# Performance work log

Hardware: AMD Instinct MI355X
Metric: run time of the kernel (lower is better)

The kernel has to match this reference:

```python
import jax, jax.numpy as jnp
import numpy as np

NUM_HEADS = 16
NUM_KV_HEADS = 4
HEAD_DIM = 128
BASE_THETA = 10000.0


def _rope_cos_sin(seq_len, head_dim, dtype):
    # standard (ntk_alpha=1) rotate-half RoPE tables: [S, head_dim]
    inv_freq = 1.0 / (BASE_THETA ** (jnp.arange(0, head_dim, 2, dtype=jnp.float32) / head_dim))
    angles = jnp.arange(seq_len, dtype=jnp.float32)[:, None] * inv_freq[None, :]  # [S, D/2]
    cos = jnp.concatenate([jnp.cos(angles), jnp.cos(angles)], axis=-1).astype(dtype)
    sin = jnp.concatenate([jnp.sin(angles), jnp.sin(angles)], axis=-1).astype(dtype)
    return cos, sin


def _rotate_half(t):
    half = t.shape[-1] // 2
    return jnp.concatenate([-t[..., half:], t[..., :half]], axis=-1)


def setup_inputs() -> dict:
    key = jax.random.key(0)
    ks = jax.random.split(key, 5)
    B, S, E = 2, 2048, 2048
    KV = NUM_KV_HEADS * HEAD_DIM  # 512
    scale = 0.02
    return {
        "x": jax.random.normal(ks[0], (B, S, E), dtype=jnp.float32),
        "Wq": jax.random.normal(ks[1], (E, E), dtype=jnp.float32) * scale,
        "Wk": jax.random.normal(ks[2], (E, KV), dtype=jnp.float32) * scale,
        "Wv": jax.random.normal(ks[3], (E, KV), dtype=jnp.float32) * scale,
        "Wo": jax.random.normal(ks[4], (E, E), dtype=jnp.float32) * scale,
    }


def reference(x, Wq, Wk, Wv, Wo):
    B, S, E = x.shape
    n_rep = NUM_HEADS // NUM_KV_HEADS
    scale = 1.0 / jnp.sqrt(jnp.float32(HEAD_DIM))

    # QKV projections (bias=False)
    q = (x @ Wq).reshape(B, S, NUM_HEADS, HEAD_DIM)
    k = (x @ Wk).reshape(B, S, NUM_KV_HEADS, HEAD_DIM)
    v = (x @ Wv).reshape(B, S, NUM_KV_HEADS, HEAD_DIM)

    # dynamic RoPE on q, k
    cos, sin = _rope_cos_sin(S, HEAD_DIM, x.dtype)
    cos = cos[None, :, None, :]
    sin = sin[None, :, None, :]
    q = q * cos + _rotate_half(q) * sin
    k = k * cos + _rotate_half(k) * sin

    # GQA: repeat kv heads to match query heads
    k = jnp.repeat(k, n_rep, axis=2)
    v = jnp.repeat(v, n_rep, axis=2)

    # [B, H, S, D]
    q = q.transpose(0, 2, 1, 3)
    k = k.transpose(0, 2, 1, 3)
    v = v.transpose(0, 2, 1, 3)

    # causal mask (window_size=0 -> standard causal, additive float mask)
    i = jnp.arange(S)[:, None]
    j = jnp.arange(S)[None, :]
    neg = jnp.finfo(jnp.float32).min
    causal = jnp.where(j > i, neg, 0.0).astype(jnp.float32)  # [S, S]

    scores = jnp.einsum("bhqd,bhkd->bhqk", q, k) * scale
    scores = scores + causal[None, None, :, :]
    weights = jax.nn.softmax(scores.astype(jnp.float32), axis=-1)
    attn = jnp.einsum("bhqk,bhkd->bhqd", weights.astype(v.dtype), v)

    attn = attn.transpose(0, 2, 1, 3).reshape(B, S, E)
    return attn @ Wo
```

## Files before the change

kernel.cpp:

```cpp
#include <hip/hip_runtime.h>
#include <math.h>


typedef __attribute__((ext_vector_type(8))) short short8;
typedef __attribute__((ext_vector_type(4))) float f32x4;
typedef __attribute__((ext_vector_type(16))) float f32x16;

typedef const __attribute__((address_space(1))) void* gvp;
typedef __attribute__((address_space(3))) void* svp;

__device__ __forceinline__ void async16(const void* g, void* l) {
  __builtin_amdgcn_global_load_lds((gvp)g, (svp)l, 16, 0, 0);
}
__device__ __forceinline__ void wait_vm0() { asm volatile("s_waitcnt vmcnt(0)" ::: "memory"); }
__device__ __forceinline__ void barrier_raw() { asm volatile("s_barrier" ::: "memory"); }

__device__ __forceinline__ unsigned short f2b(float f) {
  unsigned int u = __builtin_bit_cast(unsigned int, f);
  u += 0x7fffu + ((u >> 16) & 1u);
  return (unsigned short)(u >> 16);
}
__device__ __forceinline__ float b2f(unsigned short h) {
  unsigned int u = ((unsigned int)h) << 16;
  return __builtin_bit_cast(float, u);
}

__device__ __forceinline__ unsigned int pk_bf16(float a, float b) {
  unsigned int r;
  asm("v_cvt_pk_bf16_f32 %0, %1, %2" : "=v"(r) : "v"(a), "v"(b));
  return r;
}
__device__ __forceinline__ void plswap(unsigned int& a, unsigned int& b) {
  asm("v_permlane32_swap_b32 %0, %1" : "+v"(a), "+v"(b));
}

__global__ __launch_bounds__(256) void convx(const float* __restrict__ x,
                                             unsigned short* __restrict__ xb) {
  int i = blockIdx.x * 256 + threadIdx.x;
  const float4* p = (const float4*)x + (size_t)i * 2;
  float4 a = p[0], b4 = p[1];
  union { short8 v; unsigned short u[8]; } o;
  o.u[0] = f2b(a.x);  o.u[1] = f2b(a.y);  o.u[2] = f2b(a.z);  o.u[3] = f2b(a.w);
  o.u[4] = f2b(b4.x); o.u[5] = f2b(b4.y); o.u[6] = f2b(b4.z); o.u[7] = f2b(b4.w);
  ((short8*)xb)[i] = o.v;
}

__global__ __launch_bounds__(256) void wconv_all(const float* __restrict__ Wq,
                                                 const float* __restrict__ Wk,
                                                 const float* __restrict__ Wv,
                                                 const float* __restrict__ Wo,
                                                 unsigned short* __restrict__ WqkvT,
                                                 unsigned short* __restrict__ WoT) {
  __shared__ float t[32][33];
  int idx = blockIdx.x;
  const float* W; unsigned short* WT; int N, tx, ty;
  const int K = 2048;
  if (idx < 4096)      { W = Wq; WT = WqkvT;                         N = 2048; idx -= 0;    tx = idx & 63; ty = idx >> 6; }
  else if (idx < 5120) { W = Wk; WT = WqkvT + (size_t)2048 * 2048;   N = 512;  idx -= 4096; tx = idx & 15; ty = idx >> 4; }
  else if (idx < 6144) { W = Wv; WT = WqkvT + (size_t)2560 * 2048;   N = 512;  idx -= 5120; tx = idx & 15; ty = idx >> 4; }
  else                 { W = Wo; WT = WoT;                           N = 2048; idx -= 6144; tx = idx & 63; ty = idx >> 6; }
  int c = threadIdx.x & 31, r0 = threadIdx.x >> 5;
  int k0 = ty * 32, n0 = tx * 32;
#pragma unroll
  for (int r = r0; r < 32; r += 8) t[r][c] = W[(size_t)(k0 + r) * N + n0 + c];
  __syncthreads();
#pragma unroll
  for (int r = r0; r < 32; r += 8) WT[(size_t)(n0 + r) * K + k0 + c] = f2b(t[c][r]);
}

__global__ __launch_bounds__(256) void gemm_bt(const unsigned short* __restrict__ A,
                                               const unsigned short* __restrict__ BT,
                                               void* __restrict__ Cout,
                                               int M, int N, int K, int out_bf16) {
  const int n0 = blockIdx.x * 128;
  const int m0 = blockIdx.y * 128;
  const int tid = threadIdx.x;
  const int w = tid >> 6, lane = tid & 63, l15 = lane & 15, quad = lane >> 4;
  const int wm = w >> 1, wn = w & 1;

  __shared__ __align__(16) unsigned short As[2][128 * 64];
  __shared__ __align__(16) unsigned short Bs[2][128 * 64];

  f32x4 acc[4][4];
#pragma unroll
  for (int mi = 0; mi < 4; mi++)
#pragma unroll
    for (int ni = 0; ni < 4; ni++) acc[mi][ni] = (f32x4){0.f, 0.f, 0.f, 0.f};

  const int rl = lane >> 3;
  const int cl = lane & 7;
  const unsigned short* Ab = A + (size_t)m0 * K;
  const unsigned short* Bb = BT + (size_t)n0 * K;

#pragma unroll
  for (int i = 0; i < 4; i++) {
    int row = w * 32 + i * 8 + rl;
    int gc = cl ^ (row & 7);
    async16(Ab + (size_t)row * K + gc * 8, &As[0][(w * 32 + i * 8) * 64]);
    async16(Bb + (size_t)row * K + gc * 8, &Bs[0][(w * 32 + i * 8) * 64]);
  }

  const int nIter = K >> 6;
  for (int j = 0; j < nIter; j++) {
    wait_vm0();
    barrier_raw();
    const int cur = j & 1;

    if (j + 1 < nIter) {
      int kb = (j + 1) * 64;
#pragma unroll
      for (int i = 0; i < 4; i++) {
        int row = w * 32 + i * 8 + rl;
        int gc = cl ^ (row & 7);
        async16(Ab + (size_t)row * K + kb + gc * 8, &As[cur ^ 1][(w * 32 + i * 8) * 64]);
        async16(Bb + (size_t)row * K + kb + gc * 8, &Bs[cur ^ 1][(w * 32 + i * 8) * 64]);
      }
    }

    const unsigned short* as = &As[cur][0];
    const unsigned short* bs = &Bs[cur][0];
#pragma unroll
    for (int kk = 0; kk < 2; kk++) {
      short8 af[4], bfv[4];
#pragma unroll
      for (int mi = 0; mi < 4; mi++) {
        int row = wm * 64 + mi * 16 + l15;
        af[mi] = *(const short8*)&as[row * 64 + (((kk * 4 + quad) ^ (row & 7)) * 8)];
      }
#pragma unroll
      for (int ni = 0; ni < 4; ni++) {
        int row = wn * 64 + ni * 16 + l15;
        bfv[ni] = *(const short8*)&bs[row * 64 + (((kk * 4 + quad) ^ (row & 7)) * 8)];
      }
#pragma unroll
      for (int mi = 0; mi < 4; mi++)
#pragma unroll
        for (int ni = 0; ni < 4; ni++)
          acc[mi][ni] = __builtin_amdgcn_mfma_f32_16x16x32_bf16(af[mi], bfv[ni],
                                                                acc[mi][ni], 0, 0, 0);
    }
  }

  if (out_bf16) {
    unsigned short* C = (unsigned short*)Cout;
#pragma unroll
    for (int mi = 0; mi < 4; mi++)
#pragma unroll
      for (int ni = 0; ni < 4; ni++)
#pragma unroll
        for (int r = 0; r < 4; r++) {
          int row = m0 + wm * 64 + mi * 16 + quad * 4 + r;
          int col = n0 + wn * 64 + ni * 16 + l15;
          C[(size_t)row * N + col] = f2b(acc[mi][ni][r]);
        }
  } else {
    float* C = (float*)Cout;
#pragma unroll
    for (int mi = 0; mi < 4; mi++)
#pragma unroll
      for (int ni = 0; ni < 4; ni++)
#pragma unroll
        for (int r = 0; r < 4; r++) {
          int row = m0 + wm * 64 + mi * 16 + quad * 4 + r;
          int col = n0 + wn * 64 + ni * 16 + l15;
          C[(size_t)row * N + col] = acc[mi][ni][r];
        }
  }
}

#define SC_TOT 0.12753785056274918f
__global__ __launch_bounds__(256) void rope_kernel(const unsigned short* __restrict__ qkv,
                                                   unsigned short* __restrict__ Q,
                                                   unsigned short* __restrict__ Kd) {
  int b = blockIdx.z, hh = blockIdx.y;
  int tid = threadIdx.x;
  int d = tid & 63, sl = tid >> 6;
  int s = blockIdx.x * 4 + sl;
  const unsigned short* src = qkv + ((size_t)(b * 2048 + s)) * 3072 + hh * 128;
  float lo = b2f(src[d]), hi = b2f(src[d + 64]);
  float invf = exp2f(-0.20762050593046f * (float)d);
  float ang = (float)s * invf;
  float sn, cs;
  sincosf(ang, &sn, &cs);
  float nlo = lo * cs - hi * sn;
  float nhi = hi * cs + lo * sn;
  unsigned short* dst;
  if (hh < 16) {
    nlo *= SC_TOT; nhi *= SC_TOT;
    dst = Q + ((size_t)((b * 16 + hh) * 2048 + s)) * 128;
  } else {
    dst = Kd + ((size_t)((b * 4 + (hh - 16)) * 2048 + s)) * 128;
  }
  dst[d] = f2b(nlo);
  dst[d + 64] = f2b(nhi);
}

__global__ __launch_bounds__(256) void vtrans(const unsigned short* __restrict__ qkv,
                                              unsigned short* __restrict__ Vt) {
  int bkv = blockIdx.z;
  int b = bkv >> 2, kv = bkv & 3;
  int s0 = blockIdx.x * 64, d0 = blockIdx.y * 64;
  __shared__ unsigned short t[64][65];
  int c = threadIdx.x & 63, r0 = threadIdx.x >> 6;
  const unsigned short* src = qkv + ((size_t)(b * 2048 + s0)) * 3072 + 2560 + kv * 128 + d0;
#pragma unroll
  for (int r = r0; r < 64; r += 4) t[r][c] = src[(size_t)r * 3072 + c];
  __syncthreads();
  unsigned short* dst = Vt + ((size_t)bkv * 128 + d0) * 2048 + s0;
#pragma unroll
  for (int r = r0; r < 64; r += 4) dst[(size_t)r * 2048 + c] = t[c][r];
}

#define FIXED_M 12.0f

__device__ __forceinline__ void proc_acc(const f32x16& s, bool msk, int kvb, int q,
                                         float& l_own, short8& paL, short8& paH) {
  float p[16];
#pragma unroll
  for (int r = 0; r < 16; r++) {
    float v = exp2f(s[r] - FIXED_M);
    if (msk) {
      int kv = kvb + (r & 3) + 8 * (r >> 2);
      if (kv > q) v = 0.f;
    }
    p[r] = v;
    l_own += v;
  }
  unsigned int u0 = pk_bf16(p[0], p[1]),  u1 = pk_bf16(p[2], p[3]);
  unsigned int u2 = pk_bf16(p[4], p[5]),  u3 = pk_bf16(p[6], p[7]);
  plswap(u0, u2); plswap(u1, u3);
  unsigned int w0 = pk_bf16(p[8], p[9]),  w1 = pk_bf16(p[10], p[11]);
  unsigned int w2 = pk_bf16(p[12], p[13]), w3 = pk_bf16(p[14], p[15]);
  plswap(w0, w2); plswap(w1, w3);
  union { unsigned int u[4]; short8 s8; } a, b;
  a.u[0] = u0; a.u[1] = u1; a.u[2] = u2; a.u[3] = u3;
  b.u[0] = w0; b.u[1] = w1; b.u[2] = w2; b.u[3] = w3;
  paL = a.s8; paH = b.s8;
}

__global__ __launch_bounds__(512, 2) void flash2(const unsigned short* __restrict__ Q,
                                                 const unsigned short* __restrict__ Kc,
                                                 const unsigned short* __restrict__ Vt,
                                                 unsigned short* __restrict__ attn) {
  const int pair = blockIdx.x;
  const int h = blockIdx.y;
  const int b = blockIdx.z;
  const int kvh = h >> 2;
  const int tid = threadIdx.x;
  const int w = tid >> 6;
  const int g = w >> 2;
  const int wg = w & 3;
  const int lane = tid & 63;
  const int l31 = lane & 31, hi = lane >> 5, x7 = l31 & 7;

  __shared__ __align__(16) unsigned short kbuf[2][2][64 * 128];
  __shared__ __align__(16) unsigned short vbuf[2][2][128 * 64];
  __shared__ float lx[2][4][32];
  __shared__ float li[2][4][32];

  const unsigned short* Qb = Q  + ((size_t)(b * 16 + h)) * 2048 * 128;
  const unsigned short* Kb = Kc + ((size_t)(b * 4 + kvh)) * 2048 * 128;
  const unsigned short* Vb = Vt + ((size_t)(b * 4 + kvh)) * 128 * 2048;

  for (int t = 0; t < 2; t++) {
    const int qt = (t == 0) ? pair : (15 - pair);
    const int q0 = qt * 128;
    const int qw = q0 + wg * 32;
    const int qv = qw + l31;
    const int half = qt + 1;
    const int j0 = g * half;

    short8 qf[8];
    {
      const unsigned short* qp = Qb + (size_t)qv * 128 + hi * 8;
#pragma unroll
      for (int s = 0; s < 8; s++) qf[s] = *(const short8*)(qp + s * 16);
    }

    f32x16 o[4];
#pragma unroll
    for (int d = 0; d < 4; d++)
#pragma unroll
      for (int e = 0; e < 16; e++) o[d][e] = 0.f;
    float l_own = 0.f;

    __syncthreads();

#pragma unroll
    for (int k2 = 0; k2 < 4; k2++) {
      int m = wg * 4 + k2;
      int rl = m * 4 + (lane >> 4);
      int c8 = (lane & 15) ^ (rl & 7);
      async16(Kb + (size_t)(j0 * 64 + rl) * 128 + c8 * 8, &kbuf[g][0][m * 512]);
    }
#pragma unroll
    for (int k2 = 0; k2 < 4; k2++) {
      int m = wg * 4 + k2;
      int d = m * 8 + (lane >> 3);
      int c3 = (lane & 7) ^ (d & 7);
      async16(Vb + (size_t)d * 2048 + j0 * 64 + c3 * 8, &vbuf[g][0][m * 512]);
    }

    for (int i = 0; i < half; i++) {
      wait_vm0();
      barrier_raw();
      const int cur = i & 1;
      const int kb = (j0 + i) * 64;

      if (i + 1 < half) {
        int kb2 = kb + 64;
#pragma unroll
        for (int k2 = 0; k2 < 4; k2++) {
          int m = wg * 4 + k2;
          int rl = m * 4 + (lane >> 4);
          int c8 = (lane & 15) ^ (rl & 7);
          async16(Kb + (size_t)(kb2 + rl) * 128 + c8 * 8, &kbuf[g][cur ^ 1][m * 512]);
        }
#pragma unroll
        for (int k2 = 0; k2 < 4; k2++) {
          int m = wg * 4 + k2;
          int d = m * 8 + (lane >> 3);
          int c3 = (lane & 7) ^ (d & 7);
          async16(Vb + (size_t)d * 2048 + kb2 + c3 * 8, &vbuf[g][cur ^ 1][m * 512]);
        }
      }

      if (kb <= qw + 31) {
        f32x16 sA, sB;
#pragma unroll
        for (int e = 0; e < 16; e++) { sA[e] = 0.f; sB[e] = 0.f; }
        const unsigned short* kp = &kbuf[g][cur][0];
        __builtin_amdgcn_s_setprio(1);
#pragma unroll
        for (int s = 0; s < 8; s++) {
          int ch = (((s << 1) | hi) ^ x7) << 3;
          short8 ka = *(const short8*)&kp[l31 * 128 + ch];
          short8 kB2 = *(const short8*)&kp[(32 + l31) * 128 + ch];
          sA = __builtin_amdgcn_mfma_f32_32x32x16_bf16(ka, qf[s], sA, 0, 0, 0);
          sB = __builtin_amdgcn_mfma_f32_32x32x16_bf16(kB2, qf[s], sB, 0, 0, 0);
        }
        __builtin_amdgcn_s_setprio(0);

        const bool msk = (kb + 63 > qw);
        short8 pa[4];
        proc_acc(sA, msk, kb + 4 * hi, qv, l_own, pa[0], pa[1]);
        proc_acc(sB, msk, kb + 32 + 4 * hi, qv, l_own, pa[2], pa[3]);

        const unsigned short* vp = &vbuf[g][cur][0];
        __builtin_amdgcn_s_setprio(1);
#pragma unroll
        for (int db = 0; db < 4; db++) {
          int ro = (db * 32 + l31) * 64;
#pragma unroll
          for (int f = 0; f < 4; f++) {
            int ch = (((f << 1) | hi) ^ x7) << 3;
            short8 vf = *(const short8*)&vp[ro + ch];
            o[db] = __builtin_amdgcn_mfma_f32_32x32x16_bf16(pa[f], vf, o[db], 0, 0, 0);
          }
        }
        __builtin_amdgcn_s_setprio(0);
      }
    }

    __syncthreads();
    {
      float* wout = (float*)&kbuf[g ^ 1][0][0];
      float lown = l_own + __shfl_xor(l_own, 32);
      if (hi == 0) lx[g][wg][l31] = lown;
      const int base = wg * 2048 + lane * 4;
      if (g == 0) {
#pragma unroll
        for (int r4 = 0; r4 < 4; r4++) {
          *(f32x4*)&wout[base + 0 * 1024 + r4 * 256] =
            (f32x4){ o[2][r4 * 4 + 0], o[2][r4 * 4 + 1], o[2][r4 * 4 + 2], o[2][r4 * 4 + 3] };
          *(f32x4*)&wout[base + 1 * 1024 + r4 * 256] =
            (f32x4){ o[3][r4 * 4 + 0], o[3][r4 * 4 + 1], o[3][r4 * 4 + 2], o[3][r4 * 4 + 3] };
        }
      } else {
#pragma unroll
        for (int r4 = 0; r4 < 4; r4++) {
          *(f32x4*)&wout[base + 0 * 1024 + r4 * 256] =
            (f32x4){ o[0][r4 * 4 + 0], o[0][r4 * 4 + 1], o[0][r4 * 4 + 2], o[0][r4 * 4 + 3] };
          *(f32x4*)&wout[base + 1 * 1024 + r4 * 256] =
            (f32x4){ o[1][r4 * 4 + 0], o[1][r4 * 4 + 1], o[1][r4 * 4 + 2], o[1][r4 * 4 + 3] };
        }
      }
      __syncthreads();
      const float* rin = (const float*)&kbuf[g][0][0];
      float ltot = lown + lx[g ^ 1][wg][l31];
      if (hi == 0) li[g][wg][l31] = 1.f / ltot;
      f32x4 inv4[4];
#pragma unroll
      for (int tt = 0; tt < 4; tt++) inv4[tt] = *(const f32x4*)&li[g][wg][tt * 8 + 4 * hi];

      unsigned short* ap0 = attn + ((size_t)(b * 2048 + qw)) * 2048 + h * 128 + l31;
      if (g == 0) {
#pragma unroll
        for (int r4 = 0; r4 < 4; r4++) {
          f32x4 v0 = *(const f32x4*)&rin[base + 0 * 1024 + r4 * 256];
          f32x4 v1 = *(const f32x4*)&rin[base + 1 * 1024 + r4 * 256];
#pragma unroll
          for (int k = 0; k < 4; k++) {
            o[0][r4 * 4 + k] += v0[k];
            o[1][r4 * 4 + k] += v1[k];
          }
        }
#pragma unroll
        for (int r = 0; r < 16; r++) {
          int rowq = (r & 3) + 8 * (r >> 2) + 4 * hi;
          float iv = inv4[r >> 2][r & 3];
          ap0[(size_t)rowq * 2048 + 0]  = f2b(o[0][r] * iv);
          ap0[(size_t)rowq * 2048 + 32] = f2b(o[1][r] * iv);
        }
      } else {
#pragma unroll
        for (int r4 = 0; r4 < 4; r4++) {
          f32x4 v0 = *(const f32x4*)&rin[base + 0 * 1024 + r4 * 256];
          f32x4 v1 = *(const f32x4*)&rin[base + 1 * 1024 + r4 * 256];
#pragma unroll
          for (int k = 0; k < 4; k++) {
            o[2][r4 * 4 + k] += v0[k];
            o[3][r4 * 4 + k] += v1[k];
          }
        }
#pragma unroll
        for (int r = 0; r < 16; r++) {
          int rowq = (r & 3) + 8 * (r >> 2) + 4 * hi;
          float iv = inv4[r >> 2][r & 3];
          ap0[(size_t)rowq * 2048 + 64] = f2b(o[2][r] * iv);
          ap0[(size_t)rowq * 2048 + 96] = f2b(o[3][r] * iv);
        }
      }
    }
  }
}

extern "C" void kernel_launch(void* const* d_in, const int* in_sizes, int n_in,
                              void* d_out, int out_size, void* d_ws, size_t ws_size,
                              hipStream_t stream) {
  const float* x  = (const float*)d_in[0];
  const float* Wq = (const float*)d_in[1];
  const float* Wk = (const float*)d_in[2];
  const float* Wv = (const float*)d_in[3];
  const float* Wo = (const float*)d_in[4];
  float* out = (float*)d_out;

  char* ws = (char*)d_ws;
  unsigned short* xb    = (unsigned short*)(ws);
  unsigned short* WqkvT = (unsigned short*)(ws + 16777216);
  unsigned short* WoT   = (unsigned short*)(ws + 29360128);
  unsigned short* qkv   = (unsigned short*)(ws + 37748736);
  unsigned short* Qm    = (unsigned short*)(ws + 62914560);
  unsigned short* Km    = (unsigned short*)(ws + 79691776);
  unsigned short* Vtm   = (unsigned short*)(ws + 83886080);
  unsigned short* attn  = xb;

  convx<<<4096, 256, 0, stream>>>(x, xb);
  wconv_all<<<10240, 256, 0, stream>>>(Wq, Wk, Wv, Wo, WqkvT, WoT);

  gemm_bt<<<dim3(24, 32), 256, 0, stream>>>(xb, WqkvT, qkv, 4096, 3072, 2048, 1);

  rope_kernel<<<dim3(512, 20, 2), 256, 0, stream>>>(qkv, Qm, Km);
  vtrans<<<dim3(32, 2, 8), 256, 0, stream>>>(qkv, Vtm);

  flash2<<<dim3(8, 16, 2), 512, 0, stream>>>(Qm, Km, Vtm, attn);

  gemm_bt<<<dim3(16, 32), 256, 0, stream>>>(attn, WoT, out, 4096, 2048, 2048, 0);
}
```

Before: 312.6 us.

## Enlarge GEMM tiles to 256x256 with 8-wave ping-pong MFMA schedule

The bf16 GEMM now uses 256x256 output tiles with 512 threads (8 waves, 2x4 layout) instead of 128x128 with 4 waves. Each wave holds a 128x64 accumulator, and the inner loop runs as four quadrant phases that alternate LDS fragment loads with MFMA bursts. The bursts are separated by barriers and raised with s_setprio, so waves interleave memory and matrix work. The larger tile raises data reuse per LDS byte. The trade-off is far fewer blocks: 192 for QKV and 128 for the output projection on a 256-CU part, which may leave compute units idle. It also raises register pressure and adds extra barriers.

```diff
diff --git a/kernel.cpp b/kernel.cpp
--- a/kernel.cpp
+++ b/kernel.cpp
@@ -68,100 +68,120 @@
   for (int r = r0; r < 32; r += 8) WT[(size_t)(n0 + r) * K + k0 + c] = f2b(t[c][r]);
 }
 
-__global__ __launch_bounds__(256) void gemm_bt(const unsigned short* __restrict__ A,
-                                               const unsigned short* __restrict__ BT,
-                                               void* __restrict__ Cout,
-                                               int M, int N, int K, int out_bf16) {
-  const int n0 = blockIdx.x * 128;
-  const int m0 = blockIdx.y * 128;
+__global__ __launch_bounds__(512, 2) void gemm_bt(const unsigned short* __restrict__ A,
+                                                  const unsigned short* __restrict__ BT,
+                                                  void* __restrict__ Cout,
+                                                  int M, int N, int K, int out_bf16) {
+  const int n0 = blockIdx.x * 256;
+  const int m0 = blockIdx.y * 256;
   const int tid = threadIdx.x;
   const int w = tid >> 6, lane = tid & 63, l15 = lane & 15, quad = lane >> 4;
-  const int wm = w >> 1, wn = w & 1;
-
-  __shared__ __align__(16) unsigned short As[2][128 * 64];
-  __shared__ __align__(16) unsigned short Bs[2][128 * 64];
-
-  f32x4 acc[4][4];
-#pragma unroll
-  for (int mi = 0; mi < 4; mi++)
+  const int wm = w >> 2, wn = w & 3;
+  const int rl = lane >> 3, cl = lane & 7;
+
+  __shared__ __align__(16) unsigned short As[2][256 * 64];
+  __shared__ __align__(16) unsigned short Bs[2][256 * 64];
+
+  f32x4 acc[8][4];
+#pragma unroll
+  for (int mi = 0; mi < 8; mi++)
 #pragma unroll
     for (int ni = 0; ni < 4; ni++) acc[mi][ni] = (f32x4){0.f, 0.f, 0.f, 0.f};
 
-  const int rl = lane >> 3;
-  const int cl = lane & 7;
   const unsigned short* Ab = A + (size_t)m0 * K;
   const unsigned short* Bb = BT + (size_t)n0 * K;
 
-#pragma unroll
-  for (int i = 0; i < 4; i++) {
-    int row = w * 32 + i * 8 + rl;
-    int gc = cl ^ (row & 7);
-    async16(Ab + (size_t)row * K + gc * 8, &As[0][(w * 32 + i * 8) * 64]);
-    async16(Bb + (size_t)row * K + gc * 8, &Bs[0][(w * 32 + i * 8) * 64]);
+#define G_STAGE(KB, BUF)                                                      \
+  { _Pragma("unroll") for (int i = 0; i < 4; ++i) {                           \
+      int row = w * 32 + i * 8 + rl;                                          \
+      int gc = cl ^ (row & 7);                                                \
+      async16(Ab + (size_t)row * K + (KB) + gc * 8,                           \
+              &As[BUF][(w * 32 + i * 8) * 64]);                               \
+      async16(Bb + (size_t)row * K + (KB) + gc * 8,                           \
+              &Bs[BUF][(w * 32 + i * 8) * 64]); } }
+
+#define LOAD_A(MH)                                                            \
+  { _Pragma("unroll") for (int mi = 0; mi < 4; ++mi) {                        \
+      int row = wm * 128 + (MH) * 64 + mi * 16 + l15;                         \
+      _Pragma("unroll") for (int kk = 0; kk < 2; ++kk)                        \
+        a8[mi][kk] = *(const short8*)&as_[row * 64 +                          \
+                        (((kk * 4 + quad) ^ (row & 7)) * 8)]; } }
+
+#define LOAD_B(NH)                                                            \
+  { _Pragma("unroll") for (int ni = 0; ni < 2; ++ni) {                        \
+      int row = wn * 64 + (NH) * 32 + ni * 16 + l15;                          \
+      _Pragma("unroll") for (int kk = 0; kk < 2; ++kk)                        \
+        b4[ni][kk] = *(const short8*)&bs_[row * 64 +                          \
+                        (((kk * 4 + quad) ^ (row & 7)) * 8)]; } }
+
+#define MFMA_C(MH, NH)                                                        \
+  { __builtin_amdgcn_s_setprio(1);                                            \
+    _Pragma("unroll") for (int mi = 0; mi < 4; ++mi)                          \
+      _Pragma("unroll") for (int ni = 0; ni < 2; ++ni)                        \
+        _Pragma("unroll") for (int kk = 0; kk < 2; ++kk)                      \
+          acc[(MH) * 4 + mi][(NH) * 2 + ni] =                                 \
+            __builtin_amdgcn_mfma_f32_16x16x32_bf16(                          \
+              a8[mi][kk], b4[ni][kk],                                         \
+              acc[(MH) * 4 + mi][(NH) * 2 + ni], 0, 0, 0);                    \
+    __builtin_amdgcn_s_setprio(0); }
+
+  G_STAGE(0, 0);
+  wait_vm0();
+  barrier_raw();
+
+  const int nIter = K >> 6;
+  short8 a8[4][2], b4[2][2];
+  for (int j = 0; j < nIter; ++j) {
+    const int cur = j & 1;
+    if (j + 1 < nIter) G_STAGE((j + 1) * 64, cur ^ 1);
+    const unsigned short* as_ = &As[cur][0];
+    const unsigned short* bs_ = &Bs[cur][0];
+
+    LOAD_A(0); LOAD_B(0);
+    barrier_raw();
+    MFMA_C(0, 0);
+    barrier_raw();
+    LOAD_B(1);
+    barrier_raw();
+    MFMA_C(0, 1);
+    barrier_raw();
+    LOAD_A(1);
+    barrier_raw();
+    MFMA_C(1, 1);
+    barrier_raw();
+    LOAD_B(0);
+    barrier_raw();
+    MFMA_C(1, 0);
+    wait_vm0();
+    barrier_raw();
   }
 
-  const int nIter = K >> 6;
-  for (int j = 0; j < nIter; j++) {
-    wait_vm0();
-    barrier_raw();
-    const int cur = j & 1;
-
-    if (j + 1 < nIter) {
-      int kb = (j + 1) * 64;
-#pragma unroll
-      for (int i = 0; i < 4; i++) {
-        int row = w * 32 + i * 8 + rl;
-        int gc = cl ^ (row & 7);
-        async16(Ab + (size_t)row * K + kb + gc * 8, &As[cur ^ 1][(w * 32 + i * 8) * 64]);
-        async16(Bb + (size_t)row * K + kb + gc * 8, &Bs[cur ^ 1][(w * 32 + i * 8) * 64]);
-      }
-    }
-
-    const unsigned short* as = &As[cur][0];
-    const unsigned short* bs = &Bs[cur][0];
-#pragma unroll
-    for (int kk = 0; kk < 2; kk++) {
-      short8 af[4], bfv[4];
-#pragma unroll
-      for (int mi = 0; mi < 4; mi++) {
-        int row = wm * 64 + mi * 16 + l15;
-        af[mi] = *(const short8*)&as[row * 64 + (((kk * 4 + quad) ^ (row & 7)) * 8)];
-      }
-#pragma unroll
-      for (int ni = 0; ni < 4; ni++) {
-        int row = wn * 64 + ni * 16 + l15;
-        bfv[ni] = *(const short8*)&bs[row * 64 + (((kk * 4 + quad) ^ (row & 7)) * 8)];
-      }
-#pragma unroll
-      for (int mi = 0; mi < 4; mi++)
-#pragma unroll
-        for (int ni = 0; ni < 4; ni++)
-          acc[mi][ni] = __builtin_amdgcn_mfma_f32_16x16x32_bf16(af[mi], bfv[ni],
-                                                                acc[mi][ni], 0, 0, 0);
-    }
-  }
+#undef G_STAGE
+#undef LOAD_A
+#undef LOAD_B
+#undef MFMA_C
 
   if (out_bf16) {
     unsigned short* C = (unsigned short*)Cout;
 #pragma unroll
-    for (int mi = 0; mi < 4; mi++)
+    for (int mi = 0; mi < 8; mi++)
 #pragma unroll
       for (int ni = 0; ni < 4; ni++)
 #pragma unroll
         for (int r = 0; r < 4; r++) {
-          int row = m0 + wm * 64 + mi * 16 + quad * 4 + r;
+          int row = m0 + wm * 128 + mi * 16 + quad * 4 + r;
           int col = n0 + wn * 64 + ni * 16 + l15;
           C[(size_t)row * N + col] = f2b(acc[mi][ni][r]);
         }
   } else {
     float* C = (float*)Cout;
 #pragma unroll
-    for (int mi = 0; mi < 4; mi++)
+    for (int mi = 0; mi < 8; mi++)
 #pragma unroll
       for (int ni = 0; ni < 4; ni++)
 #pragma unroll
         for (int r = 0; r < 4; r++) {
-          int row = m0 + wm * 64 + mi * 16 + quad * 4 + r;
+          int row = m0 + wm * 128 + mi * 16 + quad * 4 + r;
           int col = n0 + wn * 64 + ni * 16 + l15;
           C[(size_t)row * N + col] = acc[mi][ni][r];
         }
@@ -458,12 +478,12 @@
   convx<<<4096, 256, 0, stream>>>(x, xb);
   wconv_all<<<10240, 256, 0, stream>>>(Wq, Wk, Wv, Wo, WqkvT, WoT);
 
-  gemm_bt<<<dim3(24, 32), 256, 0, stream>>>(xb, WqkvT, qkv, 4096, 3072, 2048, 1);
+  gemm_bt<<<dim3(12, 16), 512, 0, stream>>>(xb, WqkvT, qkv, 4096, 3072, 2048, 1);
 
   rope_kernel<<<dim3(512, 20, 2), 256, 0, stream>>>(qkv, Qm, Km);
   vtrans<<<dim3(32, 2, 8), 256, 0, stream>>>(qkv, Vtm);
 
   flash2<<<dim3(8, 16, 2), 512, 0, stream>>>(Qm, Km, Vtm, attn);
 
-  gemm_bt<<<dim3(16, 32), 256, 0, stream>>>(attn, WoT, out, 4096, 2048, 2048, 0);
-}
+  gemm_bt<<<dim3(8, 16), 512, 0, stream>>>(attn, WoT, out, 4096, 2048, 2048, 0);
+}
```

Result: slower. 351.9 us (+12.6%).

## Fuse RoPE and V transpose into QKV GEMM epilogue; merge prep kernels

Applied to the files above, without the earlier changes.

A dedicated QKV GEMM now stages its 128x128 fp32 tile in LDS and applies RoPE (for Q/K heads) or writes the transposed V layout directly. This removes the intermediate qkv buffer round trip and two separate kernel launches. The x and weight conversion kernels are also merged into one launch. The epilogue adds LDS traffic and sincos work inside the GEMM blocks. The V output is written with scattered 2-byte stores.

```diff
diff --git a/kernel.cpp b/kernel.cpp
--- a/kernel.cpp
+++ b/kernel.cpp
@@ -34,25 +34,26 @@
   asm("v_permlane32_swap_b32 %0, %1" : "+v"(a), "+v"(b));
 }
 
-__global__ __launch_bounds__(256) void convx(const float* __restrict__ x,
-                                             unsigned short* __restrict__ xb) {
-  int i = blockIdx.x * 256 + threadIdx.x;
-  const float4* p = (const float4*)x + (size_t)i * 2;
-  float4 a = p[0], b4 = p[1];
-  union { short8 v; unsigned short u[8]; } o;
-  o.u[0] = f2b(a.x);  o.u[1] = f2b(a.y);  o.u[2] = f2b(a.z);  o.u[3] = f2b(a.w);
-  o.u[4] = f2b(b4.x); o.u[5] = f2b(b4.y); o.u[6] = f2b(b4.z); o.u[7] = f2b(b4.w);
-  ((short8*)xb)[i] = o.v;
-}
-
-__global__ __launch_bounds__(256) void wconv_all(const float* __restrict__ Wq,
-                                                 const float* __restrict__ Wk,
-                                                 const float* __restrict__ Wv,
-                                                 const float* __restrict__ Wo,
-                                                 unsigned short* __restrict__ WqkvT,
-                                                 unsigned short* __restrict__ WoT) {
+__global__ __launch_bounds__(256) void prep(const float* __restrict__ x,
+                                            const float* __restrict__ Wq,
+                                            const float* __restrict__ Wk,
+                                            const float* __restrict__ Wv,
+                                            const float* __restrict__ Wo,
+                                            unsigned short* __restrict__ xb,
+                                            unsigned short* __restrict__ WqkvT,
+                                            unsigned short* __restrict__ WoT) {
   __shared__ float t[32][33];
-  int idx = blockIdx.x;
+  if (blockIdx.x < 4096) {
+    int i = blockIdx.x * 256 + threadIdx.x;
+    const float4* p = (const float4*)x + (size_t)i * 2;
+    float4 a = p[0], b4 = p[1];
+    union { short8 v; unsigned short u[8]; } o;
+    o.u[0] = f2b(a.x);  o.u[1] = f2b(a.y);  o.u[2] = f2b(a.z);  o.u[3] = f2b(a.w);
+    o.u[4] = f2b(b4.x); o.u[5] = f2b(b4.y); o.u[6] = f2b(b4.z); o.u[7] = f2b(b4.w);
+    ((short8*)xb)[i] = o.v;
+    return;
+  }
+  int idx = blockIdx.x - 4096;
   const float* W; unsigned short* WT; int N, tx, ty;
   const int K = 2048;
   if (idx < 4096)      { W = Wq; WT = WqkvT;                         N = 2048; idx -= 0;    tx = idx & 63; ty = idx >> 6; }
@@ -169,46 +170,135 @@
 }
 
 #define SC_TOT 0.12753785056274918f
-__global__ __launch_bounds__(256) void rope_kernel(const unsigned short* __restrict__ qkv,
-                                                   unsigned short* __restrict__ Q,
-                                                   unsigned short* __restrict__ Kd) {
-  int b = blockIdx.z, hh = blockIdx.y;
-  int tid = threadIdx.x;
-  int d = tid & 63, sl = tid >> 6;
-  int s = blockIdx.x * 4 + sl;
-  const unsigned short* src = qkv + ((size_t)(b * 2048 + s)) * 3072 + hh * 128;
-  float lo = b2f(src[d]), hi = b2f(src[d + 64]);
-  float invf = exp2f(-0.20762050593046f * (float)d);
-  float ang = (float)s * invf;
-  float sn, cs;
-  sincosf(ang, &sn, &cs);
-  float nlo = lo * cs - hi * sn;
-  float nhi = hi * cs + lo * sn;
-  unsigned short* dst;
-  if (hh < 16) {
-    nlo *= SC_TOT; nhi *= SC_TOT;
-    dst = Q + ((size_t)((b * 16 + hh) * 2048 + s)) * 128;
+__global__ __launch_bounds__(256) void gemm_qkv(const unsigned short* __restrict__ A,
+                                                const unsigned short* __restrict__ BT,
+                                                unsigned short* __restrict__ Qm,
+                                                unsigned short* __restrict__ Km,
+                                                unsigned short* __restrict__ Vtm) {
+  const int N = 3072, K = 2048;
+  const int n0 = blockIdx.x * 128;
+  const int m0 = blockIdx.y * 128;
+  const int tid = threadIdx.x;
+  const int w = tid >> 6, lane = tid & 63, l15 = lane & 15, quad = lane >> 4;
+  const int wm = w >> 1, wn = w & 1;
+
+  __shared__ __align__(16) unsigned char smem[65536];
+  unsigned short (*As)[128 * 64] = (unsigned short (*)[128 * 64])smem;
+  unsigned short (*Bs)[128 * 64] = (unsigned short (*)[128 * 64])(smem + 32768);
+  float* L = (float*)smem;
+
+  f32x4 acc[4][4];
+#pragma unroll
+  for (int mi = 0; mi < 4; mi++)
+#pragma unroll
+    for (int ni = 0; ni < 4; ni++) acc[mi][ni] = (f32x4){0.f, 0.f, 0.f, 0.f};
+
+  const int rl = lane >> 3;
+  const int cl = lane & 7;
+  const unsigned short* Ab = A + (size_t)m0 * K;
+  const unsigned short* Bb = BT + (size_t)n0 * K;
+
+#pragma unroll
+  for (int i = 0; i < 4; i++) {
+    int row = w * 32 + i * 8 + rl;
+    int gc = cl ^ (row & 7);
+    async16(Ab + (size_t)row * K + gc * 8, &As[0][(w * 32 + i * 8) * 64]);
+    async16(Bb + (size_t)row * K + gc * 8, &Bs[0][(w * 32 + i * 8) * 64]);
+  }
+
+  const int nIter = K >> 6;
+  for (int j = 0; j < nIter; j++) {
+    wait_vm0();
+    barrier_raw();
+    const int cur = j & 1;
+
+    if (j + 1 < nIter) {
+      int kb = (j + 1) * 64;
+#pragma unroll
+      for (int i = 0; i < 4; i++) {
+        int row = w * 32 + i * 8 + rl;
+        int gc = cl ^ (row & 7);
+        async16(Ab + (size_t)row * K + kb + gc * 8, &As[cur ^ 1][(w * 32 + i * 8) * 64]);
+        async16(Bb + (size_t)row * K + kb + gc * 8, &Bs[cur ^ 1][(w * 32 + i * 8) * 64]);
+      }
+    }
+
+    const unsigned short* as = &As[cur][0];
+    const unsigned short* bs = &Bs[cur][0];
+#pragma unroll
+    for (int kk = 0; kk < 2; kk++) {
+      short8 af[4], bfv[4];
+#pragma unroll
+      for (int mi = 0; mi < 4; mi++) {
+        int row = wm * 64 + mi * 16 + l15;
+        af[mi] = *(const short8*)&as[row * 64 + (((kk * 4 + quad) ^ (row & 7)) * 8)];
+      }
+#pragma unroll
+      for (int ni = 0; ni < 4; ni++) {
+        int row = wn * 64 + ni * 16 + l15;
+        bfv[ni] = *(const short8*)&bs[row * 64 + (((kk * 4 + quad) ^ (row & 7)) * 8)];
+      }
+#pragma unroll
+      for (int mi = 0; mi < 4; mi++)
+#pragma unroll
+        for (int ni = 0; ni < 4; ni++)
+          acc[mi][ni] = __builtin_amdgcn_mfma_f32_16x16x32_bf16(af[mi], bfv[ni],
+                                                                acc[mi][ni], 0, 0, 0);
+    }
+  }
+
+  __syncthreads();
+#pragma unroll
+  for (int mi = 0; mi < 4; mi++)
+#pragma unroll
+    for (int ni = 0; ni < 4; ni++)
+#pragma unroll
+      for (int r = 0; r < 4; r++) {
+        int rr = wm * 64 + mi * 16 + quad * 4 + r;
+        int cc = wn * 64 + ni * 16 + l15;
+        L[rr * 128 + (cc ^ (rr & 31))] = acc[mi][ni][r];
+      }
+  __syncthreads();
+
+  const int head = blockIdx.x;
+  const int b = m0 >> 11;
+  const int s_base = m0 & 2047;
+
+  if (head < 20) {
+    const int d = tid & 63, sl = tid >> 6;
+    const bool isQ = head < 16;
+    unsigned short* dq = isQ
+      ? Qm + ((size_t)((b * 16 + head) * 2048 + s_base)) * 128
+      : Km + ((size_t)((b * 4 + (head - 16)) * 2048 + s_base)) * 128;
+    const float invf = exp2f(-0.20762050593046f * (float)d);
+#pragma unroll 4
+    for (int i = 0; i < 32; i++) {
+      int s = sl + i * 4;
+      float lo = b2f(f2b(L[s * 128 + (d ^ (s & 31))]));
+      float hi = b2f(f2b(L[s * 128 + ((d + 64) ^ (s & 31))]));
+      float ang = (float)(s_base + s) * invf;
+      float sn, cs;
+      sincosf(ang, &sn, &cs);
+      float nlo = lo * cs - hi * sn;
+      float nhi = hi * cs + lo * sn;
+      if (isQ) { nlo *= SC_TOT; nhi *= SC_TOT; }
+      dq[(size_t)s * 128 + d]      = f2b(nlo);
+      dq[(size_t)s * 128 + d + 64] = f2b(nhi);
+    }
   } else {
-    dst = Kd + ((size_t)((b * 4 + (hh - 16)) * 2048 + s)) * 128;
-  }
-  dst[d] = f2b(nlo);
-  dst[d + 64] = f2b(nhi);
-}
-
-__global__ __launch_bounds__(256) void vtrans(const unsigned short* __restrict__ qkv,
-                                              unsigned short* __restrict__ Vt) {
-  int bkv = blockIdx.z;
-  int b = bkv >> 2, kv = bkv & 3;
-  int s0 = blockIdx.x * 64, d0 = blockIdx.y * 64;
-  __shared__ unsigned short t[64][65];
-  int c = threadIdx.x & 63, r0 = threadIdx.x >> 6;
-  const unsigned short* src = qkv + ((size_t)(b * 2048 + s0)) * 3072 + 2560 + kv * 128 + d0;
-#pragma unroll
-  for (int r = r0; r < 64; r += 4) t[r][c] = src[(size_t)r * 3072 + c];
-  __syncthreads();
-  unsigned short* dst = Vt + ((size_t)bkv * 128 + d0) * 2048 + s0;
-#pragma unroll
-  for (int r = r0; r < 64; r += 4) dst[(size_t)r * 2048 + c] = t[c][r];
+    const int kv = head - 20;
+    const int s_l = tid & 63, dl = tid >> 6;
+    unsigned short* dv = Vtm + ((size_t)(b * 4 + kv) * 128) * 2048;
+#pragma unroll 2
+    for (int sh = 0; sh < 2; sh++) {
+      int s = sh * 64 + s_l;
+#pragma unroll 4
+      for (int i = 0; i < 32; i++) {
+        int d = i * 4 + dl;
+        dv[(size_t)d * 2048 + s_base + s] = f2b(L[s * 128 + (d ^ (s & 31))]);
+      }
+    }
+  }
 }
 
 #define FIXED_M 12.0f
@@ -449,19 +539,14 @@
   unsigned short* xb    = (unsigned short*)(ws);
   unsigned short* WqkvT = (unsigned short*)(ws + 16777216);
   unsigned short* WoT   = (unsigned short*)(ws + 29360128);
-  unsigned short* qkv   = (unsigned short*)(ws + 37748736);
   unsigned short* Qm    = (unsigned short*)(ws + 62914560);
   unsigned short* Km    = (unsigned short*)(ws + 79691776);
   unsigned short* Vtm   = (unsigned short*)(ws + 83886080);
   unsigned short* attn  = xb;
 
-  convx<<<4096, 256, 0, stream>>>(x, xb);
-  wconv_all<<<10240, 256, 0, stream>>>(Wq, Wk, Wv, Wo, WqkvT, WoT);
-
-  gemm_bt<<<dim3(24, 32), 256, 0, stream>>>(xb, WqkvT, qkv, 4096, 3072, 2048, 1);
-
-  rope_kernel<<<dim3(512, 20, 2), 256, 0, stream>>>(qkv, Qm, Km);
-  vtrans<<<dim3(32, 2, 8), 256, 0, stream>>>(qkv, Vtm);
+  prep<<<14336, 256, 0, stream>>>(x, Wq, Wk, Wv, Wo, xb, WqkvT, WoT);
+
+  gemm_qkv<<<dim3(24, 32), 256, 0, stream>>>(xb, WqkvT, Qm, Km, Vtm);
 
   flash2<<<dim3(8, 16, 2), 512, 0, stream>>>(Qm, Km, Vtm, attn);
 
```

Measured after the change: 307.4 us. Within noise of the previous version (-1.7%).
